# Kernel tuning notes

Measured on AMD Instinct MI355X. Metric: run time of the kernel, lower is better.

## Reference

```python
import jax, jax.numpy as jnp
import numpy as np

N = 20000
E = 320000
IN_C = 256
HID = 64
OUT_C = 64
NUM_LAYERS = 3
HEADS = 8


def setup_inputs() -> dict:
    key = jax.random.key(0)
    ks = jax.random.split(key, 12)
    s_in = 1.0 / np.sqrt(IN_C)
    s_h = 1.0 / np.sqrt(HID)
    inp = {
        "x": jax.random.normal(ks[0], (N, IN_C), dtype=jnp.float32),
        "edge_index": jax.random.randint(ks[1], (2, E), 0, N, dtype=jnp.int64),
        "lin1_w": jax.random.uniform(ks[2], (IN_C, HID), jnp.float32, -s_in, s_in),
        "lin1_b": jnp.zeros((HID,), jnp.float32),
        "wq": jax.random.uniform(ks[3], (NUM_LAYERS, HID, HID), jnp.float32, -s_h, s_h),
        "bq": jnp.zeros((NUM_LAYERS, HID), jnp.float32),
        "wk": jax.random.uniform(ks[4], (NUM_LAYERS, HID, HID), jnp.float32, -s_h, s_h),
        "bk": jnp.zeros((NUM_LAYERS, HID), jnp.float32),
        "wv": jax.random.uniform(ks[5], (NUM_LAYERS, HID, HID), jnp.float32, -s_h, s_h),
        "bv": jnp.zeros((NUM_LAYERS, HID), jnp.float32),
        "lin2_w": jax.random.uniform(ks[6], (HID, OUT_C), jnp.float32, -s_h, s_h),
        "lin2_b": jnp.zeros((OUT_C,), jnp.float32),
    }
    return inp


def reference(x, edge_index, lin1_w, lin1_b, wq, bq, wk, bk, wv, bv, lin2_w, lin2_b):
    n = x.shape[0]
    C = lin1_w.shape[1]
    d = C // HEADS  # per-head dim
    inv_sqrt_d = 1.0 / (d ** 0.5)

    # gcn_norm with self-loops (symmetric normalization, edge weights = 1)
    loop = jnp.arange(n, dtype=edge_index.dtype)
    row = jnp.concatenate([edge_index[0], loop])  # source j
    col = jnp.concatenate([edge_index[1], loop])  # target i
    deg = jax.ops.segment_sum(jnp.ones_like(col, dtype=x.dtype), col, num_segments=n)
    dinv = jnp.where(deg > 0, deg ** -0.5, 0.0)
    norm = dinv[row] * dinv[col]  # [E+N]

    # input projection (dropout inactive in eval mode)
    h = jax.nn.relu(x @ lin1_w + lin1_b)
    x_all = h[:, None, :]  # [N, 1, C] growing history

    for l in range(NUM_LAYERS):
        t = x_all.shape[1]
        # node-level projections (linear commutes with gather)
        q = x_all[:, -1] @ wq[l] + bq[l]                      # [N, C]
        k = jnp.einsum("ntc,cd->ntd", x_all, wk[l]) + bk[l]   # [N, t, C]
        v = jnp.einsum("ntc,cd->ntd", x_all, wv[l]) + bv[l]   # [N, t, C]
        # per-edge multi-head attention of target's latest repr over source history
        Qe = q[col].reshape(-1, HEADS, d)                      # [E', H, d]
        Ke = k[row].reshape(-1, t, HEADS, d)                   # [E', t, H, d]
        Ve = v[row].reshape(-1, t, HEADS, d)
        scores = jnp.einsum("ehd,ethd->eht", Qe, Ke) * inv_sqrt_d
        attn = jax.nn.softmax(scores, axis=-1)                 # [E', H, t]
        msg = jnp.einsum("eht,ethd->ehd", attn, Ve).reshape(-1, C)
        msg = msg * norm[:, None]
        out = jax.ops.segment_sum(msg, col, num_segments=n)    # sum aggregation
        out = jax.nn.relu(out)
        x_all = jnp.concatenate([x_all, out[:, None, :]], axis=1)

    logits = x_all[:, -1] @ lin2_w + lin2_b
    return jax.nn.log_softmax(logits, axis=1)
```

## Files before the change

### kernel.cpp

```cpp
#include <hip/hip_runtime.h>
#include <math.h>

#define HID 64
#define HEADS 8
#define NUM_LAYERS 3

typedef __attribute__((ext_vector_type(8))) short bf16x8;
typedef __attribute__((ext_vector_type(4))) float f32x4;

__device__ __forceinline__ unsigned short f2bf(float f) {
    union { float f; unsigned int u; } cv; cv.f = f;
    unsigned int u = cv.u;
    unsigned int r = (u + 0x7FFFu + ((u >> 16) & 1u)) >> 16;
    return (unsigned short)r;
}
__device__ __forceinline__ float bflo(unsigned int u) {
    union { unsigned int u; float f; } cv; cv.u = u << 16; return cv.f;
}
__device__ __forceinline__ float bfhi(unsigned int u) {
    union { unsigned int u; float f; } cv; cv.u = u & 0xFFFF0000u; return cv.f;
}
__device__ __forceinline__ unsigned relu_pk(unsigned u) {
    unsigned m = ((u & 0x8000u) ? 0u : 0xFFFFu) |
                 ((u & 0x80000000u) ? 0u : 0xFFFF0000u);
    return u & m;
}

__global__ void k_count(const int* __restrict__ col, int* __restrict__ counts, int E) {
    int e = blockIdx.x * blockDim.x + threadIdx.x;
    if (e < E) atomicAdd(&counts[col[e]], 1);
}

__global__ __launch_bounds__(1024) void k_scan(const int* __restrict__ counts,
                                               int* __restrict__ start,
                                               float* __restrict__ dinv, int n) {
    __shared__ int wsum[16];
    __shared__ int carry_s;
    int tid = threadIdx.x;
    int lane = tid & 63, wv = tid >> 6;
    if (tid == 0) carry_s = 0;
    __syncthreads();
    for (int base = 0; base < n; base += 1024) {
        int i = base + tid;
        int v = (i < n) ? counts[i] : 0;
        int x = v;
#pragma unroll
        for (int off = 1; off < 64; off <<= 1) {
            int y = __shfl_up(x, off);
            if (lane >= off) x += y;
        }
        if (lane == 63) wsum[wv] = x;
        __syncthreads();
        if (wv == 0 && lane < 16) {
            int s = wsum[lane];
#pragma unroll
            for (int off = 1; off < 16; off <<= 1) {
                int y = __shfl_up(s, off);
                if (lane >= off) s += y;
            }
            wsum[lane] = s;
        }
        __syncthreads();
        int waveoff = (wv > 0) ? wsum[wv - 1] : 0;
        int carry = carry_s;
        if (i < n) {
            start[i] = carry + waveoff + x - v;
            dinv[i] = rsqrtf((float)(v + 1));
        }
        __syncthreads();
        if (tid == 0) carry_s = carry + wsum[15];
        __syncthreads();
    }
    if (threadIdx.x == 0) start[n] = carry_s;
}

__global__ void k_scatter(const int* __restrict__ ei, const int* __restrict__ start,
                          int* __restrict__ fill, int* __restrict__ ebuf, int E) {
    int e = blockIdx.x * blockDim.x + threadIdx.x;
    if (e >= E) return;
    int r = ei[e], c = ei[E + e];
    int pos = start[c] + atomicAdd(&fill[c], 1);
    ebuf[pos] = r;
}

#define ALD 72

__device__ __forceinline__ void stage_w_bf16(unsigned short* Wt,
                                             const float* __restrict__ w, int tid) {
    for (int idx = tid; idx < 1024; idx += 256) {
        int k = idx >> 4, n4 = (idx & 15) * 4;
        float4 wv = *(const float4*)&w[k * 64 + n4];
        Wt[(n4 + 0) * ALD + k] = f2bf(wv.x);
        Wt[(n4 + 1) * ALD + k] = f2bf(wv.y);
        Wt[(n4 + 2) * ALD + k] = f2bf(wv.z);
        Wt[(n4 + 3) * ALD + k] = f2bf(wv.w);
    }
}

__device__ __forceinline__ void mfma_step(const unsigned short* Alds,
                                          const unsigned short* Wt,
                                          int tid, f32x4 acc[4]) {
    int lane = tid & 63;
    int m0 = (tid >> 6) * 16;
    int c16 = lane & 15, quad = lane >> 4;
    const unsigned short* ar = &Alds[(m0 + c16) * ALD + quad * 8];
    bf16x8 a0 = *(const bf16x8*)ar;
    bf16x8 a1 = *(const bf16x8*)(ar + 32);
#pragma unroll
    for (int nt = 0; nt < 4; ++nt) {
        const unsigned short* br = &Wt[(nt * 16 + c16) * ALD + quad * 8];
        bf16x8 b0 = *(const bf16x8*)br;
        bf16x8 b1 = *(const bf16x8*)(br + 32);
        acc[nt] = __builtin_amdgcn_mfma_f32_16x16x32_bf16(a0, b0, acc[nt], 0, 0, 0);
        acc[nt] = __builtin_amdgcn_mfma_f32_16x16x32_bf16(a1, b1, acc[nt], 0, 0, 0);
    }
}

__global__ __launch_bounds__(256, 4) void k_lin1(const float* __restrict__ x,
                                                 const float* __restrict__ w,
                                                 const float* __restrict__ b,
                                                 unsigned short* __restrict__ h, int n) {
    __shared__ __align__(16) unsigned short Alds[64 * ALD];
    __shared__ __align__(16) unsigned short Wt[64 * ALD];
    int tid = threadIdx.x;
    int node0 = blockIdx.x * 64;
    f32x4 acc[4];
#pragma unroll
    for (int nt = 0; nt < 4; ++nt) acc[nt] = (f32x4){0.f, 0.f, 0.f, 0.f};

    for (int kc = 0; kc < 256; kc += 64) {
        __syncthreads();
        stage_w_bf16(Wt, w + kc * 64, tid);
        for (int idx = tid; idx < 1024; idx += 256) {
            int r = idx >> 4, c4 = (idx & 15) * 4;
            int node = node0 + r;
            float4 v = make_float4(0.f, 0.f, 0.f, 0.f);
            if (node < n) v = *(const float4*)&x[(size_t)node * 256 + kc + c4];
            Alds[r * ALD + c4 + 0] = f2bf(v.x);
            Alds[r * ALD + c4 + 1] = f2bf(v.y);
            Alds[r * ALD + c4 + 2] = f2bf(v.z);
            Alds[r * ALD + c4 + 3] = f2bf(v.w);
        }
        __syncthreads();
        mfma_step(Alds, Wt, tid, acc);
    }
    int lane = tid & 63;
    int m0 = (tid >> 6) * 16, c16 = lane & 15, quad = lane >> 4;
    float bias[4];
#pragma unroll
    for (int nt = 0; nt < 4; ++nt) bias[nt] = b[nt * 16 + c16];
#pragma unroll
    for (int i = 0; i < 4; ++i) {
        int node = node0 + m0 + quad * 4 + i;
        if (node < n) {
#pragma unroll
            for (int nt = 0; nt < 4; ++nt) {
                float o = acc[nt][i] + bias[nt];
                h[(size_t)node * 64 + nt * 16 + c16] = f2bf(fmaxf(o, 0.f));
            }
        }
    }
}

__global__ __launch_bounds__(256, 4) void k_qkv(
    const unsigned short* __restrict__ xsbase,
    const float* __restrict__ wq, const float* __restrict__ bq,
    const float* __restrict__ wk, const float* __restrict__ bk,
    const float* __restrict__ wv, const float* __restrict__ bv,
    float* __restrict__ q, unsigned short* __restrict__ kv,
    int n, int layer, int t, int job_offset, int kv_stride) {
    int job = blockIdx.y + job_offset;
    const unsigned short* src; const float* w; const float* b; bool relu_in;
    int kv_off = 0;
    if (job == 0) {
        src = xsbase + (size_t)layer * n * 64;
        w = wq + layer * 4096; b = bq + layer * 64;
        relu_in = (layer >= 1);
    } else if (job <= t) {
        int s = job - 1;
        src = xsbase + (size_t)s * n * 64;
        w = wk + layer * 4096; b = bk + layer * 64;
        kv_off = s * 128;
        relu_in = (s >= 1);
    } else {
        int s = job - t - 1;
        src = xsbase + (size_t)s * n * 64;
        w = wv + layer * 4096; b = bv + layer * 64;
        kv_off = (t == 1) ? 0 : s * 128 + 64;
        relu_in = (s >= 1);
    }
    __shared__ __align__(16) unsigned short Alds[64 * ALD];
    __shared__ __align__(16) unsigned short Wt[64 * ALD];
    int tid = threadIdx.x;
    int node0 = blockIdx.x * 64;
    stage_w_bf16(Wt, w, tid);
    for (int idx = tid; idx < 512; idx += 256) {
        int r = idx >> 3, seg = idx & 7;
        int node = node0 + r;
        uint4 u = make_uint4(0u, 0u, 0u, 0u);
        if (node < n) u = *(const uint4*)&src[(size_t)node * 64 + seg * 8];
        if (relu_in) {
            u.x = relu_pk(u.x); u.y = relu_pk(u.y);
            u.z = relu_pk(u.z); u.w = relu_pk(u.w);
        }
        *(uint4*)&Alds[r * ALD + seg * 8] = u;
    }
    __syncthreads();
    f32x4 acc[4];
#pragma unroll
    for (int nt = 0; nt < 4; ++nt) acc[nt] = (f32x4){0.f, 0.f, 0.f, 0.f};
    mfma_step(Alds, Wt, tid, acc);

    int lane = tid & 63;
    int m0 = (tid >> 6) * 16, c16 = lane & 15, quad = lane >> 4;
    float bias[4];
#pragma unroll
    for (int nt = 0; nt < 4; ++nt) bias[nt] = b[nt * 16 + c16];
    if (job == 0) {
#pragma unroll
        for (int i = 0; i < 4; ++i) {
            int node = node0 + m0 + quad * 4 + i;
            if (node < n) {
#pragma unroll
                for (int nt = 0; nt < 4; ++nt)
                    q[(size_t)node * 64 + nt * 16 + c16] = acc[nt][i] + bias[nt];
            }
        }
    } else {
#pragma unroll
        for (int i = 0; i < 4; ++i) {
            int node = node0 + m0 + quad * 4 + i;
            if (node < n) {
#pragma unroll
                for (int nt = 0; nt < 4; ++nt)
                    kv[(size_t)node * kv_stride + kv_off + nt * 16 + c16] =
                        f2bf(acc[nt][i] + bias[nt]);
            }
        }
    }
}

template <int T>
__global__ __launch_bounds__(256) void k_attn_g(
    const int* __restrict__ start, const int* __restrict__ ebuf,
    const float* __restrict__ dinv, const float* __restrict__ q,
    const unsigned short* __restrict__ kv, unsigned short* __restrict__ outp, int n) {
    const int KVS = (T == 1) ? 64 : T * 128;
    int node = (int)((blockIdx.x * (size_t)blockDim.x + threadIdx.x) >> 6);
    int lane = threadIdx.x & 63;
    if (node >= n) return;
    int g = lane >> 3;
    int cb = (lane & 7) * 8;
    const float isd = 0.35355339059327373f;

    float qv[8];
    if (T > 1) {
        float4 q0 = *(const float4*)&q[(size_t)node * 64 + cb];
        float4 q1 = *(const float4*)&q[(size_t)node * 64 + cb + 4];
        qv[0] = q0.x; qv[1] = q0.y; qv[2] = q0.z; qv[3] = q0.w;
        qv[4] = q1.x; qv[5] = q1.y; qv[6] = q1.z; qv[7] = q1.w;
    }
    float dc = dinv[node];
    int s0 = start[node];
    int cnt = start[node + 1] - s0 + 1;

    float acc[8];
#pragma unroll
    for (int k = 0; k < 8; ++k) acc[k] = 0.f;

    for (int base = 0; base < cnt; base += 8) {
        int idx = base + g;
        bool valid = idx < cnt;
        int r = node;
        if (valid && idx > 0) r = ebuf[s0 + idx - 1];
        float dr = valid ? dinv[r] : 0.f;
        const unsigned short* rkv = kv + (size_t)r * KVS;

        float sc[T];
        float wgt;
        if (T > 1) {
            float m = -1e30f;
#pragma unroll
            for (int s = 0; s < T; ++s) {
                uint4 ku = *(const uint4*)&rkv[s * 128 + cb];
                float p = qv[0] * bflo(ku.x) + qv[1] * bfhi(ku.x)
                        + qv[2] * bflo(ku.y) + qv[3] * bfhi(ku.y)
                        + qv[4] * bflo(ku.z) + qv[5] * bfhi(ku.z)
                        + qv[6] * bflo(ku.w) + qv[7] * bfhi(ku.w);
                p *= isd;
                sc[s] = p;
                m = fmaxf(m, p);
            }
            float denom = 0.f;
#pragma unroll
            for (int s = 0; s < T; ++s) { sc[s] = __expf(sc[s] - m); denom += sc[s]; }
            wgt = dr / denom;
        } else {
            sc[0] = 1.f;
            wgt = dr;
        }

        float mg[8];
#pragma unroll
        for (int k = 0; k < 8; ++k) mg[k] = 0.f;
#pragma unroll
        for (int s = 0; s < T; ++s) {
            uint4 vu = *(const uint4*)&rkv[((T == 1) ? 0 : s * 128 + 64) + cb];
            float wv_ = sc[s];
            mg[0] += wv_ * bflo(vu.x); mg[1] += wv_ * bfhi(vu.x);
            mg[2] += wv_ * bflo(vu.y); mg[3] += wv_ * bfhi(vu.y);
            mg[4] += wv_ * bflo(vu.z); mg[5] += wv_ * bfhi(vu.z);
            mg[6] += wv_ * bflo(vu.w); mg[7] += wv_ * bfhi(vu.w);
        }
#pragma unroll
        for (int k = 0; k < 8; ++k) acc[k] += wgt * mg[k];
    }

#pragma unroll
    for (int off = 8; off < 64; off <<= 1) {
#pragma unroll
        for (int k = 0; k < 8; ++k) acc[k] += __shfl_xor(acc[k], off);
    }
    if (g == 0) {
        ushort4 o0, o1;
        o0.x = f2bf(acc[0] * dc); o0.y = f2bf(acc[1] * dc);
        o0.z = f2bf(acc[2] * dc); o0.w = f2bf(acc[3] * dc);
        o1.x = f2bf(acc[4] * dc); o1.y = f2bf(acc[5] * dc);
        o1.z = f2bf(acc[6] * dc); o1.w = f2bf(acc[7] * dc);
        *(ushort4*)&outp[(size_t)node * 64 + cb] = o0;
        *(ushort4*)&outp[(size_t)node * 64 + cb + 4] = o1;
    }
}

__global__ __launch_bounds__(256) void k_final(
    const unsigned short* __restrict__ x3, const float* __restrict__ w,
    const float* __restrict__ b, float* __restrict__ outp, int n) {
    int wid  = (int)((blockIdx.x * (size_t)blockDim.x + threadIdx.x) >> 6);
    int lane = threadIdx.x & 63;
    if (wid >= n) return;
    float xv = fmaxf(bflo((unsigned)x3[(size_t)wid * 64 + lane]), 0.f);
    float acc = b[lane];
#pragma unroll
    for (int c = 0; c < 64; ++c) {
        float xc = __shfl(xv, c);
        acc += xc * w[c * 64 + lane];
    }
    float m = acc;
    for (int off = 1; off < 64; off <<= 1) m = fmaxf(m, __shfl_xor(m, off));
    float e = __expf(acc - m);
    float ssum = e;
    for (int off = 1; off < 64; off <<= 1) ssum += __shfl_xor(ssum, off);
    outp[(size_t)wid * 64 + lane] = acc - m - __logf(ssum);
}

extern "C" void kernel_launch(void* const* d_in, const int* in_sizes, int n_in,
                              void* d_out, int out_size, void* d_ws, size_t ws_size,
                              hipStream_t stream) {
    const float* x  = (const float*)d_in[0];
    const int*   ei = (const int*)d_in[1];
    const float* w1 = (const float*)d_in[2];
    const float* b1 = (const float*)d_in[3];
    const float* wq = (const float*)d_in[4];
    const float* bq = (const float*)d_in[5];
    const float* wk = (const float*)d_in[6];
    const float* bk = (const float*)d_in[7];
    const float* wv = (const float*)d_in[8];
    const float* bv = (const float*)d_in[9];
    const float* w2 = (const float*)d_in[10];
    const float* b2 = (const float*)d_in[11];
    float* outp = (float*)d_out;

    int n = in_sizes[0] / 256;
    int E = in_sizes[1] / 2;

    float* ws = (float*)d_ws;
    size_t off = 0;
    float* dinv = ws + off; off += (size_t)n;
    float* q    = ws + off; off += (size_t)n * 64;
    unsigned short* xsU = (unsigned short*)(ws + off); off += (size_t)n * 128;
    unsigned short* kvU = (unsigned short*)(ws + off); off += (size_t)n * 192;
    int* wsI    = (int*)(ws + off);
    int* counts = wsI;
    int* fill   = wsI + n;
    int* startA = wsI + 2 * n;
    int* ebuf   = wsI + 3 * n + 1;

    hipMemsetAsync(counts, 0, 2 * (size_t)n * sizeof(int), stream);
    k_count<<<(E + 255) / 256, 256, 0, stream>>>(ei + E, counts, E);
    k_scan<<<1, 1024, 0, stream>>>(counts, startA, dinv, n);
    k_scatter<<<(E + 255) / 256, 256, 0, stream>>>(ei, startA, fill, ebuf, E);

    k_lin1<<<(n + 63) / 64, 256, 0, stream>>>(x, w1, b1, xsU, n);

    int attn_grid = (int)(((size_t)n * 64 + 255) / 256);
    for (int l = 0; l < NUM_LAYERS; ++l) {
        int t = l + 1;
        int job_offset = (l == 0) ? 2 : 0;
        int njobs      = (l == 0) ? 1 : 1 + 2 * t;
        int kv_stride  = (t == 1) ? 64 : t * 128;
        dim3 grid((n + 63) / 64, njobs);
        k_qkv<<<grid, 256, 0, stream>>>(xsU, wq, bq, wk, bk, wv, bv,
                                        q, kvU, n, l, t, job_offset, kv_stride);
        unsigned short* dst = xsU + (size_t)(l + 1) * n * 64;
        if (t == 1)
            k_attn_g<1><<<attn_grid, 256, 0, stream>>>(startA, ebuf, dinv, q, kvU, dst, n);
        else if (t == 2)
            k_attn_g<2><<<attn_grid, 256, 0, stream>>>(startA, ebuf, dinv, q, kvU, dst, n);
        else
            k_attn_g<3><<<attn_grid, 256, 0, stream>>>(startA, ebuf, dinv, q, kvU, dst, n);
    }

    k_final<<<((int)(((long long)n * 64 + 255) / 256)), 256, 0, stream>>>(
        xsU + (size_t)NUM_LAYERS * n * 64, w2, b2, outp, n);
}
```

Baseline: 267.3 us.

## Fuse layer-0 V projection into lin1 and final linear into last attention

```diff
diff --git a/kernel.cpp b/kernel.cpp
--- a/kernel.cpp
+++ b/kernel.cpp
@@ -35,43 +35,40 @@
                                                int* __restrict__ start,
                                                float* __restrict__ dinv, int n) {
     __shared__ int wsum[16];
-    __shared__ int carry_s;
     int tid = threadIdx.x;
     int lane = tid & 63, wv = tid >> 6;
-    if (tid == 0) carry_s = 0;
+    int ipt = (n + 1023) >> 10;
+    int c0 = tid * ipt;
+    int c1 = min(n, c0 + ipt);
+    int s = 0;
+    for (int i = c0; i < c1; ++i) s += counts[i];
+    int x = s;
+#pragma unroll
+    for (int off = 1; off < 64; off <<= 1) {
+        int y = __shfl_up(x, off);
+        if (lane >= off) x += y;
+    }
+    if (lane == 63) wsum[wv] = x;
     __syncthreads();
-    for (int base = 0; base < n; base += 1024) {
-        int i = base + tid;
-        int v = (i < n) ? counts[i] : 0;
-        int x = v;
-#pragma unroll
-        for (int off = 1; off < 64; off <<= 1) {
-            int y = __shfl_up(x, off);
-            if (lane >= off) x += y;
-        }
-        if (lane == 63) wsum[wv] = x;
-        __syncthreads();
-        if (wv == 0 && lane < 16) {
-            int s = wsum[lane];
-#pragma unroll
-            for (int off = 1; off < 16; off <<= 1) {
-                int y = __shfl_up(s, off);
-                if (lane >= off) s += y;
-            }
-            wsum[lane] = s;
-        }
-        __syncthreads();
-        int waveoff = (wv > 0) ? wsum[wv - 1] : 0;
-        int carry = carry_s;
-        if (i < n) {
-            start[i] = carry + waveoff + x - v;
-            dinv[i] = rsqrtf((float)(v + 1));
-        }
-        __syncthreads();
-        if (tid == 0) carry_s = carry + wsum[15];
-        __syncthreads();
-    }
-    if (threadIdx.x == 0) start[n] = carry_s;
+    if (wv == 0 && lane < 16) {
+        int t2 = wsum[lane];
+#pragma unroll
+        for (int off = 1; off < 16; off <<= 1) {
+            int y = __shfl_up(t2, off);
+            if (lane >= off) t2 += y;
+        }
+        wsum[lane] = t2;
+    }
+    __syncthreads();
+    int waveoff = (wv > 0) ? wsum[wv - 1] : 0;
+    int run = waveoff + x - s;
+    for (int i = c0; i < c1; ++i) {
+        int v = counts[i];
+        start[i] = run;
+        dinv[i] = rsqrtf((float)(v + 1));
+        run += v;
+    }
+    if (tid == 0) start[n] = wsum[15];
 }
 
 __global__ void k_scatter(const int* __restrict__ ei, const int* __restrict__ start,
@@ -116,10 +113,11 @@
     }
 }
 
-__global__ __launch_bounds__(256, 4) void k_lin1(const float* __restrict__ x,
-                                                 const float* __restrict__ w,
-                                                 const float* __restrict__ b,
-                                                 unsigned short* __restrict__ h, int n) {
+__global__ __launch_bounds__(256, 4) void k_lin1(
+    const float* __restrict__ x, const float* __restrict__ w,
+    const float* __restrict__ b, const float* __restrict__ wv0,
+    const float* __restrict__ bv0, unsigned short* __restrict__ h,
+    unsigned short* __restrict__ kv, int n) {
     __shared__ __align__(16) unsigned short Alds[64 * ALD];
     __shared__ __align__(16) unsigned short Wt[64 * ALD];
     int tid = threadIdx.x;
@@ -149,15 +147,35 @@
     float bias[4];
 #pragma unroll
     for (int nt = 0; nt < 4; ++nt) bias[nt] = b[nt * 16 + c16];
+
+    __syncthreads();
+    stage_w_bf16(Wt, wv0, tid);
+#pragma unroll
+    for (int i = 0; i < 4; ++i) {
+        int row = m0 + quad * 4 + i;
+        int node = node0 + row;
+#pragma unroll
+        for (int nt = 0; nt < 4; ++nt) {
+            unsigned short hb = f2bf(fmaxf(acc[nt][i] + bias[nt], 0.f));
+            Alds[row * ALD + nt * 16 + c16] = hb;
+            if (node < n) h[(size_t)node * 64 + nt * 16 + c16] = hb;
+        }
+    }
+    __syncthreads();
+    f32x4 acc2[4];
+#pragma unroll
+    for (int nt = 0; nt < 4; ++nt) acc2[nt] = (f32x4){0.f, 0.f, 0.f, 0.f};
+    mfma_step(Alds, Wt, tid, acc2);
+    float bias2[4];
+#pragma unroll
+    for (int nt = 0; nt < 4; ++nt) bias2[nt] = bv0[nt * 16 + c16];
 #pragma unroll
     for (int i = 0; i < 4; ++i) {
         int node = node0 + m0 + quad * 4 + i;
         if (node < n) {
 #pragma unroll
-            for (int nt = 0; nt < 4; ++nt) {
-                float o = acc[nt][i] + bias[nt];
-                h[(size_t)node * 64 + nt * 16 + c16] = f2bf(fmaxf(o, 0.f));
-            }
+            for (int nt = 0; nt < 4; ++nt)
+                kv[(size_t)node * 64 + nt * 16 + c16] = f2bf(acc2[nt][i] + bias2[nt]);
         }
     }
 }
@@ -168,8 +186,8 @@
     const float* __restrict__ wk, const float* __restrict__ bk,
     const float* __restrict__ wv, const float* __restrict__ bv,
     float* __restrict__ q, unsigned short* __restrict__ kv,
-    int n, int layer, int t, int job_offset, int kv_stride) {
-    int job = blockIdx.y + job_offset;
+    int n, int layer, int t, int kv_stride) {
+    int job = blockIdx.y;
     const unsigned short* src; const float* w; const float* b; bool relu_in;
     int kv_off = 0;
     if (job == 0) {
@@ -186,7 +204,7 @@
         int s = job - t - 1;
         src = xsbase + (size_t)s * n * 64;
         w = wv + layer * 4096; b = bv + layer * 64;
-        kv_off = (t == 1) ? 0 : s * 128 + 64;
+        kv_off = s * 128 + 64;
         relu_in = (s >= 1);
     }
     __shared__ __align__(16) unsigned short Alds[64 * ALD];
@@ -332,25 +350,96 @@
     }
 }
 
-__global__ __launch_bounds__(256) void k_final(
-    const unsigned short* __restrict__ x3, const float* __restrict__ w,
-    const float* __restrict__ b, float* __restrict__ outp, int n) {
-    int wid  = (int)((blockIdx.x * (size_t)blockDim.x + threadIdx.x) >> 6);
+__global__ __launch_bounds__(256) void k_attn3f(
+    const int* __restrict__ start, const int* __restrict__ ebuf,
+    const float* __restrict__ dinv, const float* __restrict__ q,
+    const unsigned short* __restrict__ kv,
+    const float* __restrict__ w2, const float* __restrict__ b2,
+    float* __restrict__ outp, int n) {
+    const int T = 3, KVS = 384;
+    int node = (int)((blockIdx.x * (size_t)blockDim.x + threadIdx.x) >> 6);
     int lane = threadIdx.x & 63;
-    if (wid >= n) return;
-    float xv = fmaxf(bflo((unsigned)x3[(size_t)wid * 64 + lane]), 0.f);
-    float acc = b[lane];
+    if (node >= n) return;
+    int g = lane >> 3;
+    int cb = (lane & 7) * 8;
+    const float isd = 0.35355339059327373f;
+
+    float qv[8];
+    {
+        float4 q0 = *(const float4*)&q[(size_t)node * 64 + cb];
+        float4 q1 = *(const float4*)&q[(size_t)node * 64 + cb + 4];
+        qv[0] = q0.x; qv[1] = q0.y; qv[2] = q0.z; qv[3] = q0.w;
+        qv[4] = q1.x; qv[5] = q1.y; qv[6] = q1.z; qv[7] = q1.w;
+    }
+    float dc = dinv[node];
+    int s0 = start[node];
+    int cnt = start[node + 1] - s0 + 1;
+
+    float acc[8];
+#pragma unroll
+    for (int k = 0; k < 8; ++k) acc[k] = 0.f;
+
+    for (int base = 0; base < cnt; base += 8) {
+        int idx = base + g;
+        bool valid = idx < cnt;
+        int r = node;
+        if (valid && idx > 0) r = ebuf[s0 + idx - 1];
+        float dr = valid ? dinv[r] : 0.f;
+        const unsigned short* rkv = kv + (size_t)r * KVS;
+
+        float sc[T];
+        float m = -1e30f;
+#pragma unroll
+        for (int s = 0; s < T; ++s) {
+            uint4 ku = *(const uint4*)&rkv[s * 128 + cb];
+            float p = qv[0] * bflo(ku.x) + qv[1] * bfhi(ku.x)
+                    + qv[2] * bflo(ku.y) + qv[3] * bfhi(ku.y)
+                    + qv[4] * bflo(ku.z) + qv[5] * bfhi(ku.z)
+                    + qv[6] * bflo(ku.w) + qv[7] * bfhi(ku.w);
+            p *= isd;
+            sc[s] = p;
+            m = fmaxf(m, p);
+        }
+        float denom = 0.f;
+#pragma unroll
+        for (int s = 0; s < T; ++s) { sc[s] = __expf(sc[s] - m); denom += sc[s]; }
+        float wgt = dr / denom;
+
+        float mg[8];
+#pragma unroll
+        for (int k = 0; k < 8; ++k) mg[k] = 0.f;
+#pragma unroll
+        for (int s = 0; s < T; ++s) {
+            uint4 vu = *(const uint4*)&rkv[s * 128 + 64 + cb];
+            float wv_ = sc[s];
+            mg[0] += wv_ * bflo(vu.x); mg[1] += wv_ * bfhi(vu.x);
+            mg[2] += wv_ * bflo(vu.y); mg[3] += wv_ * bfhi(vu.y);
+            mg[4] += wv_ * bflo(vu.z); mg[5] += wv_ * bfhi(vu.z);
+            mg[6] += wv_ * bflo(vu.w); mg[7] += wv_ * bfhi(vu.w);
+        }
+#pragma unroll
+        for (int k = 0; k < 8; ++k) acc[k] += wgt * mg[k];
+    }
+
+#pragma unroll
+    for (int off = 8; off < 64; off <<= 1) {
+#pragma unroll
+        for (int k = 0; k < 8; ++k) acc[k] += __shfl_xor(acc[k], off);
+    }
+    float lg = b2[lane];
 #pragma unroll
     for (int c = 0; c < 64; ++c) {
-        float xc = __shfl(xv, c);
-        acc += xc * w[c * 64 + lane];
-    }
-    float m = acc;
-    for (int off = 1; off < 64; off <<= 1) m = fmaxf(m, __shfl_xor(m, off));
-    float e = __expf(acc - m);
+        float xc = fmaxf(__shfl(acc[c & 7], c >> 3) * dc, 0.f);
+        lg += xc * w2[c * 64 + lane];
+    }
+    float mx = lg;
+#pragma unroll
+    for (int off = 1; off < 64; off <<= 1) mx = fmaxf(mx, __shfl_xor(mx, off));
+    float e = __expf(lg - mx);
     float ssum = e;
+#pragma unroll
     for (int off = 1; off < 64; off <<= 1) ssum += __shfl_xor(ssum, off);
-    outp[(size_t)wid * 64 + lane] = acc - m - __logf(ssum);
+    outp[(size_t)node * 64 + lane] = lg - mx - __logf(ssum);
 }
 
 extern "C" void kernel_launch(void* const* d_in, const int* in_sizes, int n_in,
@@ -377,7 +466,7 @@
     size_t off = 0;
     float* dinv = ws + off; off += (size_t)n;
     float* q    = ws + off; off += (size_t)n * 64;
-    unsigned short* xsU = (unsigned short*)(ws + off); off += (size_t)n * 128;
+    unsigned short* xsU = (unsigned short*)(ws + off); off += (size_t)n * 96;
     unsigned short* kvU = (unsigned short*)(ws + off); off += (size_t)n * 192;
     int* wsI    = (int*)(ws + off);
     int* counts = wsI;
@@ -390,26 +479,24 @@
     k_scan<<<1, 1024, 0, stream>>>(counts, startA, dinv, n);
     k_scatter<<<(E + 255) / 256, 256, 0, stream>>>(ei, startA, fill, ebuf, E);
 
-    k_lin1<<<(n + 63) / 64, 256, 0, stream>>>(x, w1, b1, xsU, n);
+    k_lin1<<<(n + 63) / 64, 256, 0, stream>>>(x, w1, b1, wv, bv, xsU, kvU, n);
 
     int attn_grid = (int)(((size_t)n * 64 + 255) / 256);
-    for (int l = 0; l < NUM_LAYERS; ++l) {
-        int t = l + 1;
-        int job_offset = (l == 0) ? 2 : 0;
-        int njobs      = (l == 0) ? 1 : 1 + 2 * t;
-        int kv_stride  = (t == 1) ? 64 : t * 128;
-        dim3 grid((n + 63) / 64, njobs);
+
+    k_attn_g<1><<<attn_grid, 256, 0, stream>>>(startA, ebuf, dinv, q, kvU,
+                                               xsU + (size_t)n * 64, n);
+    {
+        dim3 grid((n + 63) / 64, 5);
         k_qkv<<<grid, 256, 0, stream>>>(xsU, wq, bq, wk, bk, wv, bv,
-                                        q, kvU, n, l, t, job_offset, kv_stride);
-        unsigned short* dst = xsU + (size_t)(l + 1) * n * 64;
-        if (t == 1)
-            k_attn_g<1><<<attn_grid, 256, 0, stream>>>(startA, ebuf, dinv, q, kvU, dst, n);
-        else if (t == 2)
-            k_attn_g<2><<<attn_grid, 256, 0, stream>>>(startA, ebuf, dinv, q, kvU, dst, n);
-        else
-            k_attn_g<3><<<attn_grid, 256, 0, stream>>>(startA, ebuf, dinv, q, kvU, dst, n);
-    }
-
-    k_final<<<((int)(((long long)n * 64 + 255) / 256)), 256, 0, stream>>>(
-        xsU + (size_t)NUM_LAYERS * n * 64, w2, b2, outp, n);
-}
+                                        q, kvU, n, 1, 2, 256);
+        k_attn_g<2><<<attn_grid, 256, 0, stream>>>(startA, ebuf, dinv, q, kvU,
+                                                   xsU + (size_t)n * 128, n);
+    }
+    {
+        dim3 grid((n + 63) / 64, 7);
+        k_qkv<<<grid, 256, 0, stream>>>(xsU, wq, bq, wk, bk, wv, bv,
+                                        q, kvU, n, 2, 3, 384);
+        k_attn3f<<<attn_grid, 256, 0, stream>>>(startA, ebuf, dinv, q, kvU,
+                                                w2, b2, outp, n);
+    }
+}
```

Measured after the change: 263.5 us. Within noise of the previous version (-1.4%).
